# Kernel optimization log

Measured on AMD Instinct MI355X. Metric: run time of the kernel, lower is better.

The kernel has to match this reference:

```python
import jax, jax.numpy as jnp
import numpy as np

L1, L2, N, C = 4096, 4096, 8, 3


def setup_inputs() -> dict:
    key = jax.random.key(0)
    k1, k2 = jax.random.split(key)
    coords1 = jax.random.uniform(k1, (L1, N, C), dtype=jnp.float32)
    coords2 = jax.random.uniform(k2, (L2, N, C), dtype=jnp.float32)
    return {"coords1": coords1, "coords2": coords2}


def reference(coords1, coords2):
    # coords1: [L1, N, C], coords2: [L2, N, C]
    l1, n, c = coords1.shape
    l2 = coords2.shape[0]
    # Batch-first layout, matching flatten_batch semantics (per-batch NN only)
    q = jnp.swapaxes(coords2, 0, 1)  # [N, L2, C] query points
    r = jnp.swapaxes(coords1, 0, 1)  # [N, L1, C] reference points
    # Squared euclidean distances per batch: [N, L2, L1]
    d2 = (
        jnp.sum(q * q, axis=-1)[:, :, None]
        + jnp.sum(r * r, axis=-1)[:, None, :]
        - 2.0 * jnp.einsum("nlc,nmc->nlm", q, r)
    )
    # tc.nearest returns global flat index; original does fmod(L1) to get the
    # per-batch index — argmin within each batch gives that directly.
    nearest = jnp.argmin(d2, axis=-1)  # [N, L2]
    clusters = nearest.T  # [L2, N]
    # torch.meshgrid(arange(L2), arange(N)) with 'ij' indexing; indices[-1] is
    # the batch index broadcast to [L2, N].
    batch_idx = jnp.broadcast_to(jnp.arange(n, dtype=jnp.int64 if False else jnp.int32), (l2, n))
    return (clusters.reshape(-1), batch_idx.reshape(-1))
```

## Files before the change

kernel.cpp:

```cpp
#include <hip/hip_runtime.h>
#include <float.h>


typedef float v2f __attribute__((ext_vector_type(2)));

constexpr int kL1 = 4096, kL2 = 4096, kN = 8;
constexpr int kChunk = 2048;
constexpr int kQPerBlock = 32;

__global__ __launch_bounds__(256, 4)
void nearest_kernel(const float* __restrict__ c1, const float* __restrict__ c2,
                    int* __restrict__ out) {
#pragma clang fp contract(off)
  __shared__ float4 refs[kChunk];

  const int tid = threadIdx.x;
  const int n = blockIdx.y;

  const int g = tid >> 4;
  const int lane16 = tid & 15;
  const int qa = blockIdx.x * kQPerBlock + g * 2;
  const int qb = qa + 1;

  const float* pa = c2 + (qa * kN + n) * 3;
  const float* pb = c2 + (qb * kN + n) * 3;
  const v2f qx = {pa[0], pb[0]};
  const v2f qy = {pa[1], pb[1]};
  const v2f qz = {pa[2], pb[2]};
  const v2f qq = {
      __fadd_rn(__fadd_rn(__fmul_rn(qx.x, qx.x), __fmul_rn(qy.x, qy.x)),
                __fmul_rn(qz.x, qz.x)),
      __fadd_rn(__fadd_rn(__fmul_rn(qx.y, qx.y), __fmul_rn(qy.y, qy.y)),
                __fmul_rn(qz.y, qz.y))};

  v2f bd0 = {FLT_MAX, FLT_MAX}, bd1 = {FLT_MAX, FLT_MAX};
  int bi0a = 0, bi0b = 0, bi1a = 0, bi1b = 0;

  for (int chunk = 0; chunk < kL1 / kChunk; ++chunk) {
    __syncthreads();

#pragma unroll
    for (int k = 0; k < kChunk / 256; ++k) {
      const int j = tid + 256 * k;
      const float* p = c1 + ((chunk * kChunk + j) * kN + n) * 3;
      const float r0 = p[0], r1 = p[1], r2 = p[2];
      const float rr = __fadd_rn(
          __fadd_rn(__fmul_rn(r0, r0), __fmul_rn(r1, r1)), __fmul_rn(r2, r2));
      refs[j] = make_float4(r0, r1, r2, rr);
    }
    __syncthreads();

    const int base = chunk * kChunk;
#pragma unroll 2
    for (int t = 0; t < kChunk / 32; ++t) {
      const int j0 = lane16 + 32 * t;
      const float4 rA = refs[j0];
      const float4 rB = refs[j0 + 16];
      {
        const v2f m0 = qx * rA.x;
        const v2f m1 = qy * rA.y;
        const v2f s01 = m0 + m1;
        const v2f m2 = qz * rA.z;
        const v2f dot = s01 + m2;
        const v2f A = qq + rA.w;
        const float da = __fmaf_rn(-2.0f, dot.x, A.x);
        const float db = __fmaf_rn(-2.0f, dot.y, A.y);
        if (da < bd0.x) { bd0.x = da; bi0a = base + j0; }
        if (db < bd0.y) { bd0.y = db; bi0b = base + j0; }
      }
      {
        const v2f m0 = qx * rB.x;
        const v2f m1 = qy * rB.y;
        const v2f s01 = m0 + m1;
        const v2f m2 = qz * rB.z;
        const v2f dot = s01 + m2;
        const v2f A = qq + rB.w;
        const float da = __fmaf_rn(-2.0f, dot.x, A.x);
        const float db = __fmaf_rn(-2.0f, dot.y, A.y);
        if (da < bd1.x) { bd1.x = da; bi1a = base + j0 + 16; }
        if (db < bd1.y) { bd1.y = db; bi1b = base + j0 + 16; }
      }
    }
  }

  float bda = bd0.x; int bia = bi0a;
  if (bd1.x < bda || (bd1.x == bda && bi1a < bia)) { bda = bd1.x; bia = bi1a; }
  float bdb = bd0.y; int bib = bi0b;
  if (bd1.y < bdb || (bd1.y == bdb && bi1b < bib)) { bdb = bd1.y; bib = bi1b; }

#pragma unroll
  for (int m = 1; m <= 8; m <<= 1) {
    const float oda = __shfl_xor(bda, m);
    const int oia = __shfl_xor(bia, m);
    if (oda < bda || (oda == bda && oia < bia)) { bda = oda; bia = oia; }
    const float odb = __shfl_xor(bdb, m);
    const int oib = __shfl_xor(bib, m);
    if (odb < bdb || (odb == bdb && oib < bib)) { bdb = odb; bib = oib; }
  }

  if (lane16 == 0) {
    out[qa * kN + n] = bia;
    out[qb * kN + n] = bib;
    out[kL2 * kN + qa * kN + n] = n;
    out[kL2 * kN + qb * kN + n] = n;
  }
}

extern "C" void kernel_launch(void* const* d_in, const int* in_sizes, int n_in,
                              void* d_out, int out_size, void* d_ws, size_t ws_size,
                              hipStream_t stream) {
  const float* c1 = (const float*)d_in[0];
  const float* c2 = (const float*)d_in[1];
  int* out = (int*)d_out;
  dim3 grid(kL2 / kQPerBlock, kN);
  nearest_kernel<<<grid, dim3(256), 0, stream>>>(c1, c2, out);
}
```

Before: 89.56 us.

## Process four queries per thread across 32-lane groups with compact loop-index tracking

Each thread now handles four query points instead of two, and each 32-lane group sweeps the reference chunk in strides of 64. Every shared-memory reference load is therefore reused across four queries, which cuts LDS traffic per distance. The thread stores only the loop counter on a new minimum and rebuilds the global index after the loop, which saves index arithmetic in the hot path. In exchange it drops packed v2f math, uses more registers for query state, and adds one more shuffle-reduction step.

```diff
diff --git a/kernel.cpp b/kernel.cpp
--- a/kernel.cpp
+++ b/kernel.cpp
@@ -2,11 +2,10 @@
 #include <float.h>
 
 
-typedef float v2f __attribute__((ext_vector_type(2)));
-
 constexpr int kL1 = 4096, kL2 = 4096, kN = 8;
 constexpr int kChunk = 2048;
 constexpr int kQPerBlock = 32;
+constexpr int kQ = 4;
 
 __global__ __launch_bounds__(256, 4)
 void nearest_kernel(const float* __restrict__ c1, const float* __restrict__ c2,
@@ -17,25 +16,25 @@
   const int tid = threadIdx.x;
   const int n = blockIdx.y;
 
-  const int g = tid >> 4;
-  const int lane16 = tid & 15;
-  const int qa = blockIdx.x * kQPerBlock + g * 2;
-  const int qb = qa + 1;
+  const int g = tid >> 5;
+  const int lane = tid & 31;
+  const int q0 = blockIdx.x * kQPerBlock + g * kQ;
 
-  const float* pa = c2 + (qa * kN + n) * 3;
-  const float* pb = c2 + (qb * kN + n) * 3;
-  const v2f qx = {pa[0], pb[0]};
-  const v2f qy = {pa[1], pb[1]};
-  const v2f qz = {pa[2], pb[2]};
-  const v2f qq = {
-      __fadd_rn(__fadd_rn(__fmul_rn(qx.x, qx.x), __fmul_rn(qy.x, qy.x)),
-                __fmul_rn(qz.x, qz.x)),
-      __fadd_rn(__fadd_rn(__fmul_rn(qx.y, qx.y), __fmul_rn(qy.y, qy.y)),
-                __fmul_rn(qz.y, qz.y))};
+  float qx[kQ], qy[kQ], qz[kQ], qq[kQ];
+#pragma unroll
+  for (int i = 0; i < kQ; ++i) {
+    const float* p = c2 + ((q0 + i) * kN + n) * 3;
+    qx[i] = p[0]; qy[i] = p[1]; qz[i] = p[2];
+    qq[i] = __fadd_rn(__fadd_rn(__fmul_rn(qx[i], qx[i]), __fmul_rn(qy[i], qy[i])),
+                      __fmul_rn(qz[i], qz[i]));
+  }
 
-  v2f bd0 = {FLT_MAX, FLT_MAX}, bd1 = {FLT_MAX, FLT_MAX};
-  int bi0a = 0, bi0b = 0, bi1a = 0, bi1b = 0;
+  float bdA[kQ], bdB[kQ];
+  int tA[kQ], tB[kQ];
+#pragma unroll
+  for (int i = 0; i < kQ; ++i) { bdA[i] = FLT_MAX; bdB[i] = FLT_MAX; tA[i] = 0; tB[i] = 0; }
 
+  int tglob = 0;
   for (int chunk = 0; chunk < kL1 / kChunk; ++chunk) {
     __syncthreads();
 
@@ -50,59 +49,52 @@
     }
     __syncthreads();
 
-    const int base = chunk * kChunk;
 #pragma unroll 2
-    for (int t = 0; t < kChunk / 32; ++t) {
-      const int j0 = lane16 + 32 * t;
-      const float4 rA = refs[j0];
-      const float4 rB = refs[j0 + 16];
-      {
-        const v2f m0 = qx * rA.x;
-        const v2f m1 = qy * rA.y;
-        const v2f s01 = m0 + m1;
-        const v2f m2 = qz * rA.z;
-        const v2f dot = s01 + m2;
-        const v2f A = qq + rA.w;
-        const float da = __fmaf_rn(-2.0f, dot.x, A.x);
-        const float db = __fmaf_rn(-2.0f, dot.y, A.y);
-        if (da < bd0.x) { bd0.x = da; bi0a = base + j0; }
-        if (db < bd0.y) { bd0.y = db; bi0b = base + j0; }
-      }
-      {
-        const v2f m0 = qx * rB.x;
-        const v2f m1 = qy * rB.y;
-        const v2f s01 = m0 + m1;
-        const v2f m2 = qz * rB.z;
-        const v2f dot = s01 + m2;
-        const v2f A = qq + rB.w;
-        const float da = __fmaf_rn(-2.0f, dot.x, A.x);
-        const float db = __fmaf_rn(-2.0f, dot.y, A.y);
-        if (da < bd1.x) { bd1.x = da; bi1a = base + j0 + 16; }
-        if (db < bd1.y) { bd1.y = db; bi1b = base + j0 + 16; }
+    for (int t2 = 0; t2 < kChunk / 64; ++t2, ++tglob) {
+      const float4 rA = refs[t2 * 64 + lane];
+      const float4 rB = refs[t2 * 64 + lane + 32];
+#pragma unroll
+      for (int i = 0; i < kQ; ++i) {
+        const float dotA = __fadd_rn(
+            __fadd_rn(__fmul_rn(qx[i], rA.x), __fmul_rn(qy[i], rA.y)),
+            __fmul_rn(qz[i], rA.z));
+        const float dA = __fmaf_rn(-2.0f, dotA, __fadd_rn(qq[i], rA.w));
+        if (dA < bdA[i]) { bdA[i] = dA; tA[i] = tglob; }
+
+        const float dotB = __fadd_rn(
+            __fadd_rn(__fmul_rn(qx[i], rB.x), __fmul_rn(qy[i], rB.y)),
+            __fmul_rn(qz[i], rB.z));
+        const float dB = __fmaf_rn(-2.0f, dotB, __fadd_rn(qq[i], rB.w));
+        if (dB < bdB[i]) { bdB[i] = dB; tB[i] = tglob; }
       }
     }
   }
 
-  float bda = bd0.x; int bia = bi0a;
-  if (bd1.x < bda || (bd1.x == bda && bi1a < bia)) { bda = bd1.x; bia = bi1a; }
-  float bdb = bd0.y; int bib = bi0b;
-  if (bd1.y < bdb || (bd1.y == bdb && bi1b < bib)) { bdb = bd1.y; bib = bi1b; }
+  float bd[kQ]; int bj[kQ];
+#pragma unroll
+  for (int i = 0; i < kQ; ++i) {
+    const int jA = tA[i] * 64 + lane;
+    const int jB = tB[i] * 64 + lane + 32;
+    bd[i] = bdA[i]; bj[i] = jA;
+    if (bdB[i] < bd[i] || (bdB[i] == bd[i] && jB < bj[i])) { bd[i] = bdB[i]; bj[i] = jB; }
+  }
 
 #pragma unroll
-  for (int m = 1; m <= 8; m <<= 1) {
-    const float oda = __shfl_xor(bda, m);
-    const int oia = __shfl_xor(bia, m);
-    if (oda < bda || (oda == bda && oia < bia)) { bda = oda; bia = oia; }
-    const float odb = __shfl_xor(bdb, m);
-    const int oib = __shfl_xor(bib, m);
-    if (odb < bdb || (odb == bdb && oib < bib)) { bdb = odb; bib = oib; }
+  for (int m = 1; m <= 16; m <<= 1) {
+#pragma unroll
+    for (int i = 0; i < kQ; ++i) {
+      const float od = __shfl_xor(bd[i], m);
+      const int oj = __shfl_xor(bj[i], m);
+      if (od < bd[i] || (od == bd[i] && oj < bj[i])) { bd[i] = od; bj[i] = oj; }
+    }
   }
 
-  if (lane16 == 0) {
-    out[qa * kN + n] = bia;
-    out[qb * kN + n] = bib;
-    out[kL2 * kN + qa * kN + n] = n;
-    out[kL2 * kN + qb * kN + n] = n;
+  if (lane == 0) {
+#pragma unroll
+    for (int i = 0; i < kQ; ++i) {
+      out[(q0 + i) * kN + n] = bj[i];
+      out[kL2 * kN + (q0 + i) * kN + n] = n;
+    }
   }
 }
 
```

Measured after the change: 93.61 us. +4.5%, slower.
